# Performance work log

Measured on AMD Instinct MI355X. Metric: run time of the kernel, lower is better.

The kernel has to match this reference:

```python
import jax, jax.numpy as jnp
import numpy as np

IH = IW = 1024          # image size (iH, iW)
NMS_CAND = 1000         # dup_attrs['nms_candidates']
NMS_THR = 0.65          # dup_attrs['nms_thr']
MAX_SEGS = 100          # max_segs


def _mask_to_box(masks):
    # masks: [N, H, W] bool -> xyxy float boxes [N, 4] in pixel coords
    N, H, W = masks.shape
    rows = masks.any(axis=2)            # [N, H]
    cols = masks.any(axis=1)            # [N, W]
    x1 = jnp.argmax(cols, axis=1)
    x2 = W - jnp.argmax(cols[:, ::-1], axis=1)
    y1 = jnp.argmax(rows, axis=1)
    y2 = H - jnp.argmax(rows[:, ::-1], axis=1)
    return jnp.stack([x1, y1, x2, y2], axis=-1).astype(jnp.float32)


def _box_iou(b):
    # b: [K, 4] xyxy -> pairwise IoU [K, K]
    x1, y1, x2, y2 = b[:, 0], b[:, 1], b[:, 2], b[:, 3]
    area = (x2 - x1) * (y2 - y1)
    ix1 = jnp.maximum(x1[:, None], x1[None, :])
    iy1 = jnp.maximum(y1[:, None], y1[None, :])
    ix2 = jnp.minimum(x2[:, None], x2[None, :])
    iy2 = jnp.minimum(y2[:, None], y2[None, :])
    inter = jnp.clip(ix2 - ix1, 0.0) * jnp.clip(iy2 - iy1, 0.0)
    union = area[:, None] + area[None, :] - inter
    return inter / jnp.maximum(union, 1e-9)


def _greedy_nms_keep(iou, thr):
    # boxes assumed pre-sorted by descending score; returns keep mask [K]
    k = iou.shape[0]
    idx = jnp.arange(k)

    def body(i, keep):
        sup = keep[i] & (iou[i] > thr) & (idx > i)
        return keep & ~sup

    return jax.lax.fori_loop(0, k, body, jnp.ones((k,), dtype=bool))


def setup_inputs() -> dict:
    key = jax.random.key(0)
    k1, k2 = jax.random.split(key)
    cls_logits = jax.random.normal(k1, (300, 81), dtype=jnp.float32)
    seg_logits = jax.random.normal(k2, (300, 200, 200), dtype=jnp.float32)
    return {"cls_logits": cls_logits, "seg_logits": seg_logits}


def reference(cls_logits, seg_logits):
    N, fH, fW = seg_logits.shape
    C = cls_logits.shape[1] - 1  # last class is background/no-object

    # mask thresholding + emptiness flag (filtering replaced by score masking)
    pred_masks = seg_logits > 0                              # [N, fH, fW]
    non_empty = pred_masks.reshape(N, -1).sum(axis=1) > 0    # [N]

    # mask -> box for NMS
    boxes = _mask_to_box(pred_masks)                         # [N, 4]

    # sigmoid scoring over (feat, class); empty masks get score -1 (never picked)
    scores = jax.nn.sigmoid(cls_logits[:, :-1])              # [N, C]
    scores = jnp.where(non_empty[:, None], scores, -1.0).reshape(-1)  # [N*C]
    feat_ids = jnp.repeat(jnp.arange(N), C)                  # [N*C]
    labels = jnp.tile(jnp.arange(C), N)                      # [N*C]

    # top nms_candidates (scores sorted descending)
    k = min(NMS_CAND, N * C)
    cand_scores, cand_ids = jax.lax.top_k(scores, k)
    cand_feats = feat_ids[cand_ids]
    cand_labels = labels[cand_ids]
    cand_boxes = boxes[cand_feats]

    # batched (class-aware) NMS: offset boxes per label
    offset = cand_labels.astype(jnp.float32)[:, None] * (float(max(fH, fW)) + 1.0)
    iou = _box_iou(cand_boxes + offset)
    keep = _greedy_nms_keep(iou, NMS_THR) & (cand_scores >= 0.0)

    # keep top max_segs among survivors
    kept_scores = jnp.where(keep, cand_scores, -jnp.inf)
    sel_scores, sel = jax.lax.top_k(kept_scores, MAX_SEGS)
    sel_feats = cand_feats[sel]
    sel_labels = cand_labels[sel]

    # upsample selected mask logits to image size and threshold
    sel_logits = seg_logits[sel_feats]                       # [M, fH, fW]
    maps = jax.image.resize(sel_logits, (MAX_SEGS, IH, IW), method='bilinear')
    out_masks = maps > 0                                     # [M, iH, iW] bool
    batch_ids = jnp.zeros((MAX_SEGS,), dtype=jnp.int32)

    return sel_labels, out_masks, sel_scores, batch_ids
```

## Files before the change

kernel.cpp:

```cpp
#include <hip/hip_runtime.h>
#include <cstdint>
#include <cstddef>

typedef unsigned int u32;
typedef unsigned long long u64;
typedef float vf4 __attribute__((ext_vector_type(4)));

#define NF 300
#define NCLS 80
#define NCLS1 81
#define FH 200
#define FW 200
#define PIX 40000
#define NC 24000
#define KCAND 1000
#define CAP 4096
#define NBINS 65536
#define MAXSEG 100
#define OUT_MASK_OFF 100
#define OUT_SCORE_OFF 104857700
#define OUT_BATCH_OFF 104857800
#define NEG_BIG -3.3895313892515355e38f
#define RYC 16

#define WS_HIST      0u
#define WS_KEYS      262144u
#define WS_COLLECT   454144u
#define WS_CNT       486912u
#define WS_BOXES     486928u
#define WS_CLAB      496928u
#define WS_CFEAT     500928u
#define WS_CSCORE    504928u
#define WS_CBOX      508928u
#define WS_ROWBITS   524928u
#define WS_SELFEAT   656128u

__device__ __forceinline__ u32 ord32_r3(float f) {
  u32 b = __float_as_uint(f);
  return (b & 0x80000000u) ? ~b : (b | 0x80000000u);
}
__device__ __forceinline__ float unord32_r3(u32 o) {
  u32 b = (o & 0x80000000u) ? (o & 0x7FFFFFFFu) : ~o;
  return __uint_as_float(b);
}

__device__ __forceinline__ float4 wcalc_r4(int i) {
  float s = __fsub_rn(__fmul_rn((float)i + 0.5f, 0.1953125f), 0.5f);
  int j0 = (int)floorf(s);
  int j1 = j0 + 1;
  float w0 = fmaxf(0.f, __fsub_rn(1.f, fabsf(__fsub_rn(s, (float)j0))));
  float w1 = fmaxf(0.f, __fsub_rn(1.f, fabsf(__fsub_rn(s, (float)j1))));
  bool in0 = (j0 >= 0) && (j0 < FH);
  bool in1 = (j1 >= 0) && (j1 < FH);
  float tot = __fadd_rn(in0 ? w0 : 0.f, in1 ? w1 : 0.f);
  float w0n = in0 ? (w0 / tot) : 0.f;
  float w1n = in1 ? (w1 / tot) : 0.f;
  return make_float4(w0n, w1n, (float)max(j0, 0), (float)min(j1, FH - 1));
}

__global__ void r5_init(u32* __restrict__ hist, u32* __restrict__ cnts) {
  int i = blockIdx.x * 256 + threadIdx.x;
  hist[i] = 0u;
  if (i < 4) cnts[i] = 0u;
}

__global__ void r5_boxes(const float* __restrict__ seg, const float* __restrict__ cls,
                         float4* __restrict__ boxes, u64* __restrict__ keys,
                         u32* __restrict__ hist) {
  __shared__ int sminx[256], sminy[256], smaxx[256], smaxy[256];
  int n = blockIdx.x, t = threadIdx.x;
  const float4* img = (const float4*)(seg + (size_t)n * PIX);
  int minx = FW, miny = FH, maxx = -1, maxy = -1;
  for (int q = t; q < PIX / 4; q += 256) {
    float4 v = img[q];
    int p = q * 4;
    int y = p / FW;
    int x = p - y * FW;
    if (v.x > 0.f) { minx = min(minx, x);     maxx = max(maxx, x);     miny = min(miny, y); maxy = max(maxy, y); }
    if (v.y > 0.f) { minx = min(minx, x + 1); maxx = max(maxx, x + 1); miny = min(miny, y); maxy = max(maxy, y); }
    if (v.z > 0.f) { minx = min(minx, x + 2); maxx = max(maxx, x + 2); miny = min(miny, y); maxy = max(maxy, y); }
    if (v.w > 0.f) { minx = min(minx, x + 3); maxx = max(maxx, x + 3); miny = min(miny, y); maxy = max(maxy, y); }
  }
  sminx[t] = minx; sminy[t] = miny; smaxx[t] = maxx; smaxy[t] = maxy;
  __syncthreads();
  for (int s = 128; s > 0; s >>= 1) {
    if (t < s) {
      sminx[t] = min(sminx[t], sminx[t + s]);
      sminy[t] = min(sminy[t], sminy[t + s]);
      smaxx[t] = max(smaxx[t], smaxx[t + s]);
      smaxy[t] = max(smaxy[t], smaxy[t + s]);
    }
    __syncthreads();
  }
  bool ne = smaxx[0] >= 0;
  if (t == 0) {
    float4 b;
    if (ne) b = make_float4((float)sminx[0], (float)sminy[0], (float)(smaxx[0] + 1), (float)(smaxy[0] + 1));
    else    b = make_float4(0.f, 0.f, (float)FW, (float)FH);
    boxes[n] = b;
  }
  if (t < NCLS) {
    float sc;
    if (ne) {
      float lg = cls[n * NCLS1 + t];
      sc = 1.0f / (1.0f + expf(-lg));
    } else {
      sc = -1.0f;
    }
    u32 o = ord32_r3(sc);
    u32 i = (u32)(n * NCLS + t);
    keys[i] = ((u64)o << 32) | (u64)(0xFFFFFFFFu - i);
    atomicAdd(&hist[o >> 16], 1u);
  }
}

__global__ void r6_thresh(const u32* __restrict__ hist, u32* __restrict__ cnts) {
  __shared__ u32 s[1024];
  int t = threadIdx.x;
  const uint4* hp = (const uint4*)(hist) + t * 16;
  u32 sum = 0;
  #pragma unroll
  for (int b = 0; b < 16; b++) {
    uint4 v = hp[b];
    sum += v.x + v.y + v.z + v.w;
  }
  s[t] = sum;
  __syncthreads();
  for (int off = 1; off < 1024; off <<= 1) {
    u32 v = s[t];
    u32 o = (t + off < 1024) ? s[t + off] : 0u;
    __syncthreads();
    s[t] = v + o;
    __syncthreads();
  }
  u32 sufnext = (t < 1023) ? s[t + 1] : 0u;
  if (s[t] >= (u32)KCAND && sufnext < (u32)KCAND) {
    u32 run = sufnext;
    u32 B = (u32)(t * 64);
    for (int b = 63; b >= 0; b--) {
      run += hist[t * 64 + b];
      if (run >= (u32)KCAND) { B = (u32)(t * 64 + b); break; }
    }
    cnts[1] = B;
  }
}

__global__ void r5_collect(const u64* __restrict__ keys, const u32* __restrict__ cnts,
                           u64* __restrict__ collect, u32* __restrict__ counter) {
  int i = blockIdx.x * 256 + threadIdx.x;
  u32 B = cnts[1];
  bool pass = false;
  u64 k = 0ull;
  if (i < NC) {
    k = keys[i];
    pass = ((u32)(k >> 48) >= B);
  }
  u64 m = __ballot(pass);
  int lane = threadIdx.x & 63;
  u32 base = 0u;
  if (lane == 0 && m) base = atomicAdd(counter, (u32)__popcll(m));
  base = __shfl(base, 0, 64);
  if (pass) {
    u32 pos = base + (u32)__popcll(m & ((1ull << lane) - 1ull));
    if (pos < CAP) collect[pos] = k;
  }
}

__global__ void r5_rank(const u64* __restrict__ collect, const u32* __restrict__ cnts,
                        const float4* __restrict__ boxes,
                        int* __restrict__ clab, int* __restrict__ cfeat,
                        float* __restrict__ cscore, float4* __restrict__ cbox) {
  __shared__ u64 sk[CAP];
  int M = min((int)cnts[0], CAP);
  int t = threadIdx.x;
  for (int j = t; j < M; j += 256) sk[j] = collect[j];
  __syncthreads();
  int j = blockIdx.x * 256 + t;
  if (j < M) {
    u64 my = sk[j];
    int r = 0;
    for (int k = 0; k < M; k++) r += (sk[k] > my) ? 1 : 0;
    if (r < KCAND) {
      u32 idx = 0xFFFFFFFFu - (u32)(my & 0xFFFFFFFFull);
      int n = (int)idx / NCLS, c = (int)idx - n * NCLS;
      clab[r] = c;
      cfeat[r] = n;
      cscore[r] = unord32_r3((u32)(my >> 32));
      float4 b = boxes[n];
      float off = (float)c * 201.0f;
      cbox[r] = make_float4(b.x + off, b.y + off, b.z + off, b.w + off);
    }
  }
}

__global__ void r7_iou(const float4* __restrict__ cbox, u64* __restrict__ rowT) {
  __shared__ float4 sb[KCAND];
  int t = threadIdx.x;
  for (int j = t; j < KCAND; j += 256) sb[j] = cbox[j];
  __syncthreads();
  int w = t >> 6, lane = t & 63;
  int i = blockIdx.x * 4 + w;
  float4 bi = make_float4(0.f, 0.f, 0.f, 0.f);
  float ai = 0.f;
  if (i < KCAND) { bi = sb[i]; ai = (bi.z - bi.x) * (bi.w - bi.y); }
  for (int ch = 0; ch < 16; ch++) {
    int j = ch * 64 + lane;
    bool pred = false;
    if (i < KCAND && j < KCAND && j > i) {
      float4 bj = sb[j];
      float aj = (bj.z - bj.x) * (bj.w - bj.y);
      float ix1 = fmaxf(bi.x, bj.x), iy1 = fmaxf(bi.y, bj.y);
      float ix2 = fminf(bi.z, bj.z), iy2 = fminf(bi.w, bj.w);
      float inter = fmaxf(ix2 - ix1, 0.f) * fmaxf(iy2 - iy1, 0.f);
      float uni = ai + aj - inter;
      float iou = inter / fmaxf(uni, 1e-9f);
      pred = iou > 0.65f;
    }
    u64 m = __ballot(pred);
    if (lane == 0) rowT[(size_t)ch * 1024 + i] = m;
  }
}

__global__ void r7_nms_sel(const u64* __restrict__ rowT, const float* __restrict__ cscore,
                           const int* __restrict__ clab, const int* __restrict__ cfeat,
                           float* __restrict__ out, int* __restrict__ selfeat) {
  __shared__ u64 sup[16];
  __shared__ u64 keep[16];
  __shared__ u64 sel[16];
  __shared__ u32 pre[17];
  int t = threadIdx.x;
  int wv = t >> 6, lane = t & 63;
  if (t < 16) sup[t] = 0ull;
  __syncthreads();
  for (int c = 0; c < 16; c++) {
    u64 row = 0ull;
    if (wv > c) row = rowT[(size_t)wv * 1024 + c * 64 + lane];
    if (wv == 0) {
      u64 r = rowT[(size_t)c * 1024 + c * 64 + lane];
      u64 s = sup[c];
      u64 k = 0ull;
      #pragma unroll
      for (int b = 0; b < 64; b++) {
        u64 rb = __shfl(r, b, 64);
        if (!((s >> b) & 1ull)) { s |= rb; k |= (1ull << b); }
      }
      if (lane == 0) keep[c] = k;
    }
    __syncthreads();
    if (wv > c) {
      u64 kk = keep[c];
      u64 acc = ((kk >> lane) & 1ull) ? row : 0ull;
      #pragma unroll
      for (int off = 32; off >= 1; off >>= 1) acc |= __shfl_xor(acc, off, 64);
      if (lane == 0) sup[wv] |= acc;
    }
    __syncthreads();
  }
  {
    bool s = false;
    if (t < KCAND) {
      bool kp = ((keep[t >> 6] >> (t & 63)) & 1ull) != 0ull;
      s = kp && (cscore[t] >= 0.f);
    }
    u64 m = __ballot(s);
    if (lane == 0) sel[wv] = m;
  }
  __syncthreads();
  if (t == 0) {
    u32 acc = 0;
    #pragma unroll
    for (int c = 0; c < 16; c++) { pre[c] = acc; acc += (u32)__popcll(sel[c]); }
    pre[16] = acc;
  }
  __syncthreads();
  u32 nkept = pre[16];
  if (t < KCAND) {
    int j = t;
    u64 w = sel[j >> 6];
    bool s = ((w >> (j & 63)) & 1ull) != 0ull;
    u32 below = pre[j >> 6] + (u32)__popcll(w & ((1ull << (j & 63)) - 1ull));
    u32 r = s ? below : (nkept + (u32)j - below);
    if (r < MAXSEG) {
      out[r] = (float)clab[j];
      out[OUT_SCORE_OFF + r] = s ? cscore[j] : NEG_BIG;
      out[OUT_BATCH_OFF + r] = 0.0f;
      selfeat[r] = cfeat[j];
    }
  }
}

__global__ void __launch_bounds__(256) r4_resize(const float* __restrict__ seg,
                                                 const int* __restrict__ selfeat,
                                                 float* __restrict__ outm) {
  __shared__ float srow[6][FW];
  int t = threadIdx.x;
  int yb = blockIdx.x * RYC, slot = blockIdx.y;
  int feat = selfeat[slot];
  const float* img = seg + (size_t)feat * PIX;
  float4 wxa = wcalc_r4(t * 4), wxb = wcalc_r4(t * 4 + 1),
         wxc = wcalc_r4(t * 4 + 2), wxd = wcalc_r4(t * 4 + 3);
  int ylo = (int)wcalc_r4(yb).z;
  int yhi = (int)wcalc_r4(yb + RYC - 1).w;
  int nr = yhi - ylo + 1;
  for (int e = t; e < nr * FW; e += 256) {
    int rr = e / FW, cc = e - rr * FW;
    srow[rr][cc] = img[(ylo + rr) * FW + cc];
  }
  __syncthreads();
  int xb = t * 4;
  int xa0 = (int)wxa.z, xa1 = (int)wxa.w;
  int xb0 = (int)wxb.z, xb1 = (int)wxb.w;
  int xc0 = (int)wxc.z, xc1 = (int)wxc.w;
  int xd0 = (int)wxd.z, xd1 = (int)wxd.w;
  float* obase = outm + (size_t)slot * 1048576 + (size_t)yb * 1024 + xb;
  #pragma unroll
  for (int r = 0; r < RYC; r++) {
    float4 wy = wcalc_r4(yb + r);
    const float* r0 = srow[(int)wy.z - ylo];
    const float* r1 = srow[(int)wy.w - ylo];
    float wy0 = wy.x, wy1 = wy.y;
    float ta0 = __fmaf_rn(wy1, r1[xa0], __fmul_rn(wy0, r0[xa0]));
    float ta1 = __fmaf_rn(wy1, r1[xa1], __fmul_rn(wy0, r0[xa1]));
    float va  = __fmaf_rn(wxa.y, ta1, __fmul_rn(wxa.x, ta0));
    float tb0 = __fmaf_rn(wy1, r1[xb0], __fmul_rn(wy0, r0[xb0]));
    float tb1 = __fmaf_rn(wy1, r1[xb1], __fmul_rn(wy0, r0[xb1]));
    float vb  = __fmaf_rn(wxb.y, tb1, __fmul_rn(wxb.x, tb0));
    float tc0 = __fmaf_rn(wy1, r1[xc0], __fmul_rn(wy0, r0[xc0]));
    float tc1 = __fmaf_rn(wy1, r1[xc1], __fmul_rn(wy0, r0[xc1]));
    float vc  = __fmaf_rn(wxc.y, tc1, __fmul_rn(wxc.x, tc0));
    float td0 = __fmaf_rn(wy1, r1[xd0], __fmul_rn(wy0, r0[xd0]));
    float td1 = __fmaf_rn(wy1, r1[xd1], __fmul_rn(wy0, r0[xd1]));
    float vd  = __fmaf_rn(wxd.y, td1, __fmul_rn(wxd.x, td0));
    vf4 res;
    res.x = (va > 0.0f) ? 1.0f : 0.0f;
    res.y = (vb > 0.0f) ? 1.0f : 0.0f;
    res.z = (vc > 0.0f) ? 1.0f : 0.0f;
    res.w = (vd > 0.0f) ? 1.0f : 0.0f;
    *(vf4*)(obase + (size_t)r * 1024) = res;
  }
}

extern "C" void kernel_launch(void* const* d_in, const int* in_sizes, int n_in,
                              void* d_out, int out_size, void* d_ws, size_t ws_size,
                              hipStream_t stream) {
  const float* cls = (const float*)d_in[0];
  const float* seg = (const float*)d_in[1];
  float* out = (float*)d_out;
  char* ws = (char*)d_ws;

  u32* hist      = (u32*)(ws + WS_HIST);
  u64* keys      = (u64*)(ws + WS_KEYS);
  u64* collect   = (u64*)(ws + WS_COLLECT);
  u32* cnts      = (u32*)(ws + WS_CNT);
  float4* boxes  = (float4*)(ws + WS_BOXES);
  int* clab      = (int*)(ws + WS_CLAB);
  int* cfeat     = (int*)(ws + WS_CFEAT);
  float* cscore  = (float*)(ws + WS_CSCORE);
  float4* cbox   = (float4*)(ws + WS_CBOX);
  u64* rowT      = (u64*)(ws + WS_ROWBITS);
  int* selfeat   = (int*)(ws + WS_SELFEAT);

  r5_init<<<dim3(NBINS / 256), dim3(256), 0, stream>>>(hist, cnts);
  r5_boxes<<<dim3(NF), dim3(256), 0, stream>>>(seg, cls, boxes, keys, hist);
  r6_thresh<<<dim3(1), dim3(1024), 0, stream>>>(hist, cnts);
  r5_collect<<<dim3((NC + 255) / 256), dim3(256), 0, stream>>>(keys, cnts, collect, &cnts[0]);
  r5_rank<<<dim3(16), dim3(256), 0, stream>>>(collect, cnts, boxes, clab, cfeat, cscore, cbox);
  r7_iou<<<dim3(256), dim3(256), 0, stream>>>(cbox, rowT);
  r7_nms_sel<<<dim3(1), dim3(1024), 0, stream>>>(rowT, cscore, clab, cfeat, out, selfeat);
  r4_resize<<<dim3(1024 / RYC, MAXSEG), dim3(256), 0, stream>>>(seg, selfeat, out + OUT_MASK_OFF);
}
```

Baseline: 559.0 us.

## Fuse threshold, collect and rank kernels into one single-block select kernel

Merges the histogram threshold search, candidate compaction and rank-by-counting into one 1024-thread block kernel that keeps the collected keys in shared memory and counts them with a shared atomic. This removes two kernel launches, the global collect buffer and the global counter and its initialisation. In exchange the O(M^2) ranking now runs on a single block instead of 16 blocks, which could lengthen that phase when many keys pass the threshold.

```diff
diff --git a/kernel.cpp b/kernel.cpp
--- a/kernel.cpp
+++ b/kernel.cpp
@@ -25,8 +25,6 @@
 
 #define WS_HIST      0u
 #define WS_KEYS      262144u
-#define WS_COLLECT   454144u
-#define WS_CNT       486912u
 #define WS_BOXES     486928u
 #define WS_CLAB      496928u
 #define WS_CFEAT     500928u
@@ -58,10 +56,9 @@
   return make_float4(w0n, w1n, (float)max(j0, 0), (float)min(j1, FH - 1));
 }
 
-__global__ void r5_init(u32* __restrict__ hist, u32* __restrict__ cnts) {
+__global__ void r8_init(u32* __restrict__ hist) {
   int i = blockIdx.x * 256 + threadIdx.x;
   hist[i] = 0u;
-  if (i < 4) cnts[i] = 0u;
 }
 
 __global__ void r5_boxes(const float* __restrict__ seg, const float* __restrict__ cls,
@@ -114,9 +111,15 @@
   }
 }
 
-__global__ void r6_thresh(const u32* __restrict__ hist, u32* __restrict__ cnts) {
-  __shared__ u32 s[1024];
+__global__ void r8_select(const u32* __restrict__ hist, const u64* __restrict__ keys,
+                          const float4* __restrict__ boxes,
+                          int* __restrict__ clab, int* __restrict__ cfeat,
+                          float* __restrict__ cscore, float4* __restrict__ cbox) {
+  __shared__ u32 ssum[1024];
+  __shared__ u64 sk[CAP];
+  __shared__ u32 sB, scnt;
   int t = threadIdx.x;
+  if (t == 0) scnt = 0u;
   const uint4* hp = (const uint4*)(hist) + t * 16;
   u32 sum = 0;
   #pragma unroll
@@ -124,59 +127,43 @@
     uint4 v = hp[b];
     sum += v.x + v.y + v.z + v.w;
   }
-  s[t] = sum;
+  ssum[t] = sum;
   __syncthreads();
   for (int off = 1; off < 1024; off <<= 1) {
-    u32 v = s[t];
-    u32 o = (t + off < 1024) ? s[t + off] : 0u;
-    __syncthreads();
-    s[t] = v + o;
-    __syncthreads();
-  }
-  u32 sufnext = (t < 1023) ? s[t + 1] : 0u;
-  if (s[t] >= (u32)KCAND && sufnext < (u32)KCAND) {
+    u32 v = ssum[t];
+    u32 o = (t + off < 1024) ? ssum[t + off] : 0u;
+    __syncthreads();
+    ssum[t] = v + o;
+    __syncthreads();
+  }
+  u32 sufnext = (t < 1023) ? ssum[t + 1] : 0u;
+  if (ssum[t] >= (u32)KCAND && sufnext < (u32)KCAND) {
     u32 run = sufnext;
     u32 B = (u32)(t * 64);
     for (int b = 63; b >= 0; b--) {
       run += hist[t * 64 + b];
       if (run >= (u32)KCAND) { B = (u32)(t * 64 + b); break; }
     }
-    cnts[1] = B;
-  }
-}
-
-__global__ void r5_collect(const u64* __restrict__ keys, const u32* __restrict__ cnts,
-                           u64* __restrict__ collect, u32* __restrict__ counter) {
-  int i = blockIdx.x * 256 + threadIdx.x;
-  u32 B = cnts[1];
-  bool pass = false;
-  u64 k = 0ull;
-  if (i < NC) {
-    k = keys[i];
-    pass = ((u32)(k >> 48) >= B);
-  }
-  u64 m = __ballot(pass);
-  int lane = threadIdx.x & 63;
-  u32 base = 0u;
-  if (lane == 0 && m) base = atomicAdd(counter, (u32)__popcll(m));
-  base = __shfl(base, 0, 64);
-  if (pass) {
-    u32 pos = base + (u32)__popcll(m & ((1ull << lane) - 1ull));
-    if (pos < CAP) collect[pos] = k;
-  }
-}
-
-__global__ void r5_rank(const u64* __restrict__ collect, const u32* __restrict__ cnts,
-                        const float4* __restrict__ boxes,
-                        int* __restrict__ clab, int* __restrict__ cfeat,
-                        float* __restrict__ cscore, float4* __restrict__ cbox) {
-  __shared__ u64 sk[CAP];
-  int M = min((int)cnts[0], CAP);
-  int t = threadIdx.x;
-  for (int j = t; j < M; j += 256) sk[j] = collect[j];
-  __syncthreads();
-  int j = blockIdx.x * 256 + t;
-  if (j < M) {
+    sB = B;
+  }
+  __syncthreads();
+  u32 B = sB;
+  int lane = t & 63;
+  for (int i = t; i < NC; i += 1024) {
+    u64 k = keys[i];
+    bool pass = ((u32)(k >> 48) >= B);
+    u64 m = __ballot(pass);
+    u32 base = 0u;
+    if (lane == 0 && m) base = atomicAdd(&scnt, (u32)__popcll(m));
+    base = __shfl(base, 0, 64);
+    if (pass) {
+      u32 pos = base + (u32)__popcll(m & ((1ull << lane) - 1ull));
+      if (pos < CAP) sk[pos] = k;
+    }
+  }
+  __syncthreads();
+  int M = min((int)scnt, CAP);
+  for (int j = t; j < M; j += 1024) {
     u64 my = sk[j];
     int r = 0;
     for (int k = 0; k < M; k++) r += (sk[k] > my) ? 1 : 0;
@@ -350,8 +337,6 @@
 
   u32* hist      = (u32*)(ws + WS_HIST);
   u64* keys      = (u64*)(ws + WS_KEYS);
-  u64* collect   = (u64*)(ws + WS_COLLECT);
-  u32* cnts      = (u32*)(ws + WS_CNT);
   float4* boxes  = (float4*)(ws + WS_BOXES);
   int* clab      = (int*)(ws + WS_CLAB);
   int* cfeat     = (int*)(ws + WS_CFEAT);
@@ -360,11 +345,9 @@
   u64* rowT      = (u64*)(ws + WS_ROWBITS);
   int* selfeat   = (int*)(ws + WS_SELFEAT);
 
-  r5_init<<<dim3(NBINS / 256), dim3(256), 0, stream>>>(hist, cnts);
+  r8_init<<<dim3(NBINS / 256), dim3(256), 0, stream>>>(hist);
   r5_boxes<<<dim3(NF), dim3(256), 0, stream>>>(seg, cls, boxes, keys, hist);
-  r6_thresh<<<dim3(1), dim3(1024), 0, stream>>>(hist, cnts);
-  r5_collect<<<dim3((NC + 255) / 256), dim3(256), 0, stream>>>(keys, cnts, collect, &cnts[0]);
-  r5_rank<<<dim3(16), dim3(256), 0, stream>>>(collect, cnts, boxes, clab, cfeat, cscore, cbox);
+  r8_select<<<dim3(1), dim3(1024), 0, stream>>>(hist, keys, boxes, clab, cfeat, cscore, cbox);
   r7_iou<<<dim3(256), dim3(256), 0, stream>>>(cbox, rowT);
   r7_nms_sel<<<dim3(1), dim3(1024), 0, stream>>>(rowT, cscore, clab, cfeat, out, selfeat);
   r4_resize<<<dim3(1024 / RYC, MAXSEG), dim3(256), 0, stream>>>(seg, selfeat, out + OUT_MASK_OFF);
```

New measurement: 574.5 us. +2.8%, slower.
